# Optimization experiments

Hardware: AMD Instinct MI355X
Metric: run time of the kernel (lower is better)

The kernel has to match this reference:

```python
import jax, jax.numpy as jnp
import numpy as np

N = 50000      # nodes
E = 800000     # edges (avg degree 16)
LM = 768       # lm_input_dim
H = 192        # hidden_dim = 32*6
B6 = 32        # per-branch dim = hidden_dim/6
SLOPE = 0.01   # nn.LeakyReLU default negative slope


def setup_inputs() -> dict:
    key = jax.random.key(0)
    ks = jax.random.split(key, 32)
    f = lambda i, shape, s=0.05: (jax.random.normal(ks[i], shape, jnp.float32) * s)
    inp = {
        "pre_x": f(0, (N, LM)),
        "x": f(1, (N, LM)),
        "edge_index": jax.random.randint(ks[2], (2, E), 0, N),
        "edge_type": jax.random.randint(ks[3], (E,), 0, 3),
        "num_prop": f(4, (N, 5)),
        "num_category": f(5, (N, 1)),
        "des_tensor": f(6, (N, LM)),
        "tweet_tensor": f(7, (N, LM)),
        # parameters (torch nn.Linear convention: W is [out, in], y = x @ W.T + b)
        "W_des": f(8, (B6, LM)), "b_des": f(9, (B6,)),
        "W_tweet": f(10, (B6, LM)), "b_tweet": f(11, (B6,)),
        "W_tweet_tr": f(12, (B6, LM)), "b_tweet_tr": f(13, (B6,)),
        "W_prop": f(14, (B6, 5)), "b_prop": f(15, (B6,)),
        "W_cat": f(16, (B6, 1)), "b_cat": f(17, (B6,)),
        "W_text": f(18, (B6, LM)), "b_text": f(19, (B6,)),
        "W_in": f(20, (H, H)), "b_in": f(21, (H,)),
        "W_c1": f(22, (H, H)), "b_c1": f(23, (H,)),
        "W_c2": f(24, (H, H)), "b_c2": f(25, (H,)),
        "W_o1": f(26, (96, H)), "b_o1": f(27, (96,)),
        "W_o2": f(28, (2, 96)), "b_o2": f(29, (2,)),
    }
    return inp


def _gcn_conv(h, W, b, src, dst):
    """PyG GCNConv: symmetric-normalized aggregation with added self-loops.
    out[v] = sum_{u->v} (d_u d_v)^{-1/2} (h_u W^T) + (1/d_v) (h_v W^T) + b
    where d includes the self-loop (+1)."""
    n = h.shape[0]
    hW = h @ W.T                                                  # [N, H]
    deg = jax.ops.segment_sum(jnp.ones(src.shape[0], h.dtype), dst,
                              num_segments=n) + 1.0               # [N]
    dinv = jax.lax.rsqrt(deg)
    norm = dinv[src] * dinv[dst]                                  # [E]
    agg = jax.ops.segment_sum(hW[src] * norm[:, None], dst,
                              num_segments=n)                     # [N, H]
    return agg + hW * (1.0 / deg)[:, None] + b


def reference(pre_x, x, edge_index, edge_type, num_prop, num_category,
              des_tensor, tweet_tensor,
              W_des, b_des, W_tweet, b_tweet, W_tweet_tr, b_tweet_tr,
              W_prop, b_prop, W_cat, b_cat, W_text, b_text,
              W_in, b_in, W_c1, b_c1, W_c2, b_c2,
              W_o1, b_o1, W_o2, b_o2):
    lrelu = lambda v: jax.nn.leaky_relu(v, SLOPE)
    branch = lambda t, W, b: lrelu(t @ W.T + b)   # dropout is identity in eval

    d = branch(des_tensor, W_des, b_des)
    pre_t = branch(pre_x, W_tweet, b_tweet)
    t = branch(x, W_tweet_tr, b_tweet_tr)
    n = branch(num_prop, W_prop, b_prop)
    c = branch(num_category, W_cat, b_cat)
    tw = branch(tweet_tensor, W_text, b_text)

    h = jnp.concatenate((n, c, d, tw, pre_t, t), axis=1)          # [N, 192]
    h = lrelu(h @ W_in.T + b_in)

    src, dst = edge_index[0], edge_index[1]
    h = _gcn_conv(h, W_c1, b_c1, src, dst)
    h = _gcn_conv(h, W_c2, b_c2, src, dst)

    em = lrelu(h @ W_o1.T + b_o1)                                 # [N, 96]
    out = em @ W_o2.T + b_o2                                      # [N, 2]
    return (out, em)
```

## Files before the change

kernel.cpp:

```cpp
#include <hip/hip_runtime.h>

#define NN 50000
#define EE 800000
#define LMD 768
#define HD 192
#define SLOPE 0.01f

typedef short bf16x8 __attribute__((ext_vector_type(8)));
typedef float f32x4 __attribute__((ext_vector_type(4)));
typedef unsigned short u16;

__device__ __forceinline__ float lrelu(float v){ return v > 0.f ? v : SLOPE * v; }

__device__ __forceinline__ u16 f2bf(float f){
    unsigned u = __float_as_uint(f);
    u += 0x7FFF + ((u >> 16) & 1u);
    return (u16)(u >> 16);
}
__device__ __forceinline__ float bf2f(u16 v){
    return __uint_as_float(((unsigned)v) << 16);
}
__device__ __forceinline__ bf16x8 as_bf8(float4 v){
    union { float4 f; bf16x8 b; } u; u.f = v; return u.b;
}

__global__ __launch_bounds__(256) void k_prep(
    const float* __restrict__ W0, const float* __restrict__ W1,
    const float* __restrict__ W2, const float* __restrict__ W3,
    const float* __restrict__ Win, const float* __restrict__ Wc1,
    const float* __restrict__ Wc2, const float* __restrict__ Wo1,
    u16* __restrict__ out)
{
    int m = blockIdx.y;
    int idx = blockIdx.x * 256 + threadIdx.x;
    const float* src; int nelem; int K;
    switch (m) {
      case 0: src = W0;  nelem = 32*768;  K = 768; break;
      case 1: src = W1;  nelem = 32*768;  K = 768; break;
      case 2: src = W2;  nelem = 32*768;  K = 768; break;
      case 3: src = W3;  nelem = 32*768;  K = 768; break;
      case 4: src = Win; nelem = 192*192; K = 192; break;
      case 5: src = Wc1; nelem = 192*192; K = 192; break;
      case 6: src = Wc2; nelem = 192*192; K = 192; break;
      default: src = Wo1; nelem = 96*192; K = 192; break;
    }
    if (idx >= nelem) return;
    u16 v = f2bf(src[idx]);
    int c = idx / K, k = idx - c * K;
    int cb = c >> 4, lr = c & 15;
    int sg = k >> 5, kk = k & 31, hi = kk >> 3, j = kk & 7;
    int lane = hi * 16 + lr;
    size_t dst;
    if (m < 4)      dst = (size_t)m * 24576 + (sg * 2 + cb) * 512 + lane * 8 + j;
    else if (m < 7) dst = 98304 + (size_t)(m - 4) * 36864 + (sg * 12 + cb) * 512 + lane * 8 + j;
    else            dst = 208896 + (size_t)(sg * 6 + cb) * 512 + lane * 8 + j;
    out[dst] = v;
}

__global__ __launch_bounds__(256, 3) void k_branch(
    const float* __restrict__ des, const float* __restrict__ twt,
    const float* __restrict__ prex, const float* __restrict__ xx,
    const u16* __restrict__ Wf,
    const float* __restrict__ bd, const float* __restrict__ btx,
    const float* __restrict__ btw, const float* __restrict__ btr,
    u16* __restrict__ h)
{
    __shared__ u16 Abuf[16][776];
    __shared__ float scr[4][16][32];

    const int br = blockIdx.y;
    const float* A; const float* bias; int colBase;
    switch (br) {
      case 0:  A = des;  bias = bd;  colBase = 64;  break;
      case 1:  A = twt;  bias = btx; colBase = 96;  break;
      case 2:  A = prex; bias = btw; colBase = 128; break;
      default: A = xx;   bias = btr; colBase = 160; break;
    }

    const int t0 = threadIdx.x, w = t0 >> 6, l = t0 & 63;
    const int hi = l >> 4, lr = l & 15;

    bf16x8 Bfr[12];
    {
        const u16* wp = Wf + br * 24576;
        #pragma unroll
        for (int cc = 0; cc < 6; ++cc)
            #pragma unroll
            for (int cb = 0; cb < 2; ++cb)
                Bfr[cc * 2 + cb] = *(const bf16x8*)(wp + ((w * 6 + cc) * 2 + cb) * 512 + l * 8);
    }

    const int rrow = t0 >> 4;
    const int col0 = (t0 & 15) * 2;
    const float bias0 = bias[col0], bias1 = bias[col0 + 1];

    float4 f4[12];
    int tile = blockIdx.x;
    {
        const float* ab = A + (size_t)tile * 12288 + w * 3072 + l * 4;
        #pragma unroll
        for (int i = 0; i < 12; ++i) f4[i] = *(const float4*)(ab + i * 256);
    }

    for (; tile < 3125; tile += 192) {
        asm volatile("s_waitcnt vmcnt(0)" ::: "memory");
        #pragma unroll
        for (int i = 0; i < 12; ++i) {
            const int rr = i / 3, third = i % 3;
            unsigned plo = (unsigned)f2bf(f4[i].x) | ((unsigned)f2bf(f4[i].y) << 16);
            unsigned phi = (unsigned)f2bf(f4[i].z) | ((unsigned)f2bf(f4[i].w) << 16);
            uint2 pk; pk.x = plo; pk.y = phi;
            *(uint2*)&Abuf[w * 4 + rr][third * 256 + l * 4] = pk;
        }
        const int tnext = tile + 192;
        if (tnext < 3125) {
            const float* ab = A + (size_t)tnext * 12288 + w * 3072 + l * 4;
            #pragma unroll
            for (int i = 0; i < 12; ++i) f4[i] = *(const float4*)(ab + i * 256);
        }
        __syncthreads();

        f32x4 acc[2] = {};
        #pragma unroll
        for (int cc = 0; cc < 6; ++cc) {
            const int cg = w * 6 + cc;
            bf16x8 af = *(const bf16x8*)&Abuf[lr][cg * 32 + hi * 8];
            acc[0] = __builtin_amdgcn_mfma_f32_16x16x32_bf16(af, Bfr[cc * 2 + 0], acc[0], 0, 0, 0);
            acc[1] = __builtin_amdgcn_mfma_f32_16x16x32_bf16(af, Bfr[cc * 2 + 1], acc[1], 0, 0, 0);
        }
        #pragma unroll
        for (int cb = 0; cb < 2; ++cb)
            #pragma unroll
            for (int rg = 0; rg < 4; ++rg)
                scr[w][hi * 4 + rg][cb * 16 + lr] = acc[cb][rg];
        __syncthreads();

        float2 s; s.x = 0.f; s.y = 0.f;
        #pragma unroll
        for (int ww = 0; ww < 4; ++ww) {
            float2 p = *(const float2*)&scr[ww][rrow][col0];
            s.x += p.x; s.y += p.y;
        }
        float v0 = lrelu(s.x + bias0);
        float v1 = lrelu(s.y + bias1);
        unsigned pk = (unsigned)f2bf(v0) | ((unsigned)f2bf(v1) << 16);
        *(unsigned*)&h[((size_t)tile * 16 + rrow) * HD + colBase + col0] = pk;
    }
}

template<bool BIAS, bool LRELU>
__global__ __launch_bounds__(512) void k_hgemm(
    const u16* __restrict__ A, const u16* __restrict__ Wf,
    const float* __restrict__ bias, u16* __restrict__ out)
{
    __shared__ u16 Bs[36864];
    const int t = threadIdx.x, w = t >> 6, l = t & 63;
    const int hi = l >> 4, lr = l & 15;
    const int rowBase = blockIdx.x * 128;
    {
        const uint4* s_ = (const uint4*)Wf; uint4* d_ = (uint4*)Bs;
        #pragma unroll
        for (int i = 0; i < 9; ++i) d_[i * 512 + t] = s_[i * 512 + t];
    }
    int r0 = rowBase + w * 16 + lr;
    int rowc = r0 < NN ? r0 : NN - 1;
    const u16* ap = A + (size_t)rowc * HD;
    float4 araw[6];
    #pragma unroll
    for (int sg = 0; sg < 6; ++sg) {
        araw[sg] = *(const float4*)(ap + sg * 32 + hi * 8);
        asm volatile("" :: "v"(araw[sg].x), "v"(araw[sg].y), "v"(araw[sg].z), "v"(araw[sg].w));
    }
    __syncthreads();

    f32x4 acc[12] = {};
    #pragma unroll
    for (int sg = 0; sg < 6; ++sg) {
        bf16x8 af = as_bf8(araw[sg]);
        #pragma unroll
        for (int cb = 0; cb < 12; ++cb) {
            bf16x8 bf = *(const bf16x8*)(Bs + (sg * 12 + cb) * 512 + l * 8);
            acc[cb] = __builtin_amdgcn_mfma_f32_16x16x32_bf16(af, bf, acc[cb], 0, 0, 0);
        }
    }

    #pragma unroll
    for (int cb = 0; cb < 12; ++cb) {
        int cl = cb * 16 + lr;
        float bv = BIAS ? bias[cl] : 0.f;
        #pragma unroll
        for (int rg = 0; rg < 4; ++rg) {
            int r = rowBase + w * 16 + hi * 4 + rg;
            if (r < NN) {
                float v = acc[cb][rg] + bv;
                if (LRELU) v = lrelu(v);
                out[(size_t)r * HD + cl] = f2bf(v);
            }
        }
    }
}

__global__ __launch_bounds__(512) void k_final(
    const u16* __restrict__ A, const u16* __restrict__ Wf,
    const float* __restrict__ b1, const float* __restrict__ W2,
    const float* __restrict__ b2, float* __restrict__ em, float* __restrict__ out)
{
    __shared__ u16 Bs[18432];
    const int t = threadIdx.x, w = t >> 6, l = t & 63;
    const int hi = l >> 4, lr = l & 15;
    const int rowBase = blockIdx.x * 128;
    {
        const uint4* s_ = (const uint4*)Wf; uint4* d_ = (uint4*)Bs;
        #pragma unroll
        for (int i = 0; i < 5; ++i) { int idx = i * 512 + t; if (idx < 2304) d_[idx] = s_[idx]; }
    }
    int r0 = rowBase + w * 16 + lr;
    int rowc = r0 < NN ? r0 : NN - 1;
    const u16* ap = A + (size_t)rowc * HD;
    float4 araw[6];
    #pragma unroll
    for (int sg = 0; sg < 6; ++sg) {
        araw[sg] = *(const float4*)(ap + sg * 32 + hi * 8);
        asm volatile("" :: "v"(araw[sg].x), "v"(araw[sg].y), "v"(araw[sg].z), "v"(araw[sg].w));
    }
    __syncthreads();

    f32x4 acc[6] = {};
    #pragma unroll
    for (int sg = 0; sg < 6; ++sg) {
        bf16x8 af = as_bf8(araw[sg]);
        #pragma unroll
        for (int cb = 0; cb < 6; ++cb) {
            bf16x8 bf = *(const bf16x8*)(Bs + (sg * 6 + cb) * 512 + l * 8);
            acc[cb] = __builtin_amdgcn_mfma_f32_16x16x32_bf16(af, bf, acc[cb], 0, 0, 0);
        }
    }

    float w2v[2][6], bv[6];
    #pragma unroll
    for (int cb = 0; cb < 6; ++cb) {
        bv[cb] = b1[cb * 16 + lr];
        w2v[0][cb] = W2[cb * 16 + lr];
        w2v[1][cb] = W2[96 + cb * 16 + lr];
    }

    #pragma unroll
    for (int rg = 0; rg < 4; ++rg) {
        int r = rowBase + w * 16 + hi * 4 + rg;
        float o0 = 0.f, o1 = 0.f;
        #pragma unroll
        for (int cb = 0; cb < 6; ++cb) {
            float v = lrelu(acc[cb][rg] + bv[cb]);
            if (r < NN) em[(size_t)r * 96 + cb * 16 + lr] = v;
            o0 += v * w2v[0][cb];
            o1 += v * w2v[1][cb];
        }
        #pragma unroll
        for (int d = 1; d < 16; d <<= 1) {
            o0 += __shfl_xor(o0, d);
            o1 += __shfl_xor(o1, d);
        }
        if (lr == 0 && r < NN) {
            out[r * 2 + 0] = o0 + b2[0];
            out[r * 2 + 1] = o1 + b2[1];
        }
    }
}

__global__ __launch_bounds__(256) void k_small_branch(
    const float* __restrict__ nprop, const float* __restrict__ ncat,
    const float* __restrict__ Wp, const float* __restrict__ bp,
    const float* __restrict__ Wc, const float* __restrict__ bc,
    u16* __restrict__ h)
{
    int idx = blockIdx.x * 256 + threadIdx.x;
    if (idx >= NN * 64) return;
    int row = idx >> 6, c = idx & 63;
    float acc;
    if (c < 32) {
        acc = bp[c];
        #pragma unroll
        for (int k = 0; k < 5; ++k) acc += nprop[row * 5 + k] * Wp[c * 5 + k];
    } else {
        int cc = c - 32;
        acc = bc[cc] + ncat[row] * Wc[cc];
    }
    h[(size_t)row * HD + c] = f2bf(lrelu(acc));
}

__global__ void k_count(const int* __restrict__ ei, int* __restrict__ deg)
{
    int e = blockIdx.x * 256 + threadIdx.x;
    if (e < EE) atomicAdd(&deg[ei[EE + e]], 1);
}

__global__ void k_deginv(const int* __restrict__ deg, float* __restrict__ dinv, float* __restrict__ invdeg)
{
    int v = blockIdx.x * 256 + threadIdx.x;
    if (v < NN) {
        float d = (float)(deg[v] + 1);
        dinv[v] = rsqrtf(d);
        invdeg[v] = 1.0f / d;
    }
}

__global__ __launch_bounds__(1024) void k_scan1(const int* __restrict__ deg, int* __restrict__ rp, int* __restrict__ part)
{
    __shared__ int sh[1024];
    int tid = threadIdx.x, i = blockIdx.x * 1024 + tid;
    int x = (i < NN) ? deg[i] : 0;
    sh[tid] = x;
    __syncthreads();
    for (int off = 1; off < 1024; off <<= 1) {
        int y = (tid >= off) ? sh[tid - off] : 0;
        __syncthreads();
        sh[tid] += y;
        __syncthreads();
    }
    if (i < NN) rp[i] = sh[tid] - x;
    if (tid == 1023) part[blockIdx.x] = sh[tid];
}

__global__ void k_scan2(int* part, int nb, int* rp)
{
    if (threadIdx.x == 0 && blockIdx.x == 0) {
        int run = 0;
        for (int b = 0; b < nb; ++b) { int t = part[b]; part[b] = run; run += t; }
        rp[NN] = run;
    }
}

__global__ void k_scan3(int* rp, const int* __restrict__ part)
{
    int i = blockIdx.x * 256 + threadIdx.x;
    if (i < NN) rp[i] += part[i >> 10];
}

__global__ void k_fill(const int* __restrict__ ei, const float* __restrict__ dinv,
                       int* __restrict__ cursor, int* __restrict__ cs, float* __restrict__ nrm)
{
    int e = blockIdx.x * 256 + threadIdx.x;
    if (e >= EE) return;
    int s = ei[e], d = ei[EE + e];
    int pos = atomicAdd(&cursor[d], 1);
    cs[pos] = s;
    nrm[pos] = dinv[s] * dinv[d];
}

__global__ __launch_bounds__(240) void k_agg(const u16* __restrict__ hW,
    const int* __restrict__ rp, const int* __restrict__ cs, const float* __restrict__ nrm,
    const float* __restrict__ invdeg, const float* __restrict__ bias, u16* __restrict__ out)
{
    int v = blockIdx.x * 5 + threadIdx.y;
    int f0 = threadIdx.x * 4;
    int s0 = rp[v], s1 = rp[v + 1];
    float4 bv = *reinterpret_cast<const float4*>(bias + f0);
    ushort4 hv = *reinterpret_cast<const ushort4*>(hW + (size_t)v * HD + f0);
    float idg = invdeg[v];
    float a0 = bf2f(hv.x) * idg + bv.x;
    float a1 = bf2f(hv.y) * idg + bv.y;
    float a2 = bf2f(hv.z) * idg + bv.z;
    float a3 = bf2f(hv.w) * idg + bv.w;
    int i = s0;
    for (; i + 4 <= s1; i += 4) {
        int c0 = cs[i], c1 = cs[i+1], c2 = cs[i+2], c3 = cs[i+3];
        float n0 = nrm[i], n1 = nrm[i+1], n2 = nrm[i+2], n3 = nrm[i+3];
        ushort4 g0 = *reinterpret_cast<const ushort4*>(hW + (size_t)c0 * HD + f0);
        ushort4 g1 = *reinterpret_cast<const ushort4*>(hW + (size_t)c1 * HD + f0);
        ushort4 g2 = *reinterpret_cast<const ushort4*>(hW + (size_t)c2 * HD + f0);
        ushort4 g3 = *reinterpret_cast<const ushort4*>(hW + (size_t)c3 * HD + f0);
        a0 += bf2f(g0.x) * n0; a1 += bf2f(g0.y) * n0; a2 += bf2f(g0.z) * n0; a3 += bf2f(g0.w) * n0;
        a0 += bf2f(g1.x) * n1; a1 += bf2f(g1.y) * n1; a2 += bf2f(g1.z) * n1; a3 += bf2f(g1.w) * n1;
        a0 += bf2f(g2.x) * n2; a1 += bf2f(g2.y) * n2; a2 += bf2f(g2.z) * n2; a3 += bf2f(g2.w) * n2;
        a0 += bf2f(g3.x) * n3; a1 += bf2f(g3.y) * n3; a2 += bf2f(g3.z) * n3; a3 += bf2f(g3.w) * n3;
    }
    for (; i < s1; ++i) {
        int c = cs[i]; float n = nrm[i];
        ushort4 g = *reinterpret_cast<const ushort4*>(hW + (size_t)c * HD + f0);
        a0 += bf2f(g.x) * n; a1 += bf2f(g.y) * n; a2 += bf2f(g.z) * n; a3 += bf2f(g.w) * n;
    }
    ushort4 o;
    o.x = f2bf(a0); o.y = f2bf(a1); o.z = f2bf(a2); o.w = f2bf(a3);
    *reinterpret_cast<ushort4*>(out + (size_t)v * HD + f0) = o;
}

extern "C" void kernel_launch(void* const* d_in, const int* in_sizes, int n_in,
                              void* d_out, int out_size, void* d_ws, size_t ws_size,
                              hipStream_t stream)
{
    const float* pre_x = (const float*)d_in[0];
    const float* x     = (const float*)d_in[1];
    const int*   ei    = (const int*)d_in[2];
    const float* nprop = (const float*)d_in[4];
    const float* ncat  = (const float*)d_in[5];
    const float* des   = (const float*)d_in[6];
    const float* twt   = (const float*)d_in[7];
    const float* W_des  = (const float*)d_in[8],  *b_des  = (const float*)d_in[9];
    const float* W_tw   = (const float*)d_in[10], *b_tw   = (const float*)d_in[11];
    const float* W_tr   = (const float*)d_in[12], *b_tr   = (const float*)d_in[13];
    const float* W_prop = (const float*)d_in[14], *b_prop = (const float*)d_in[15];
    const float* W_cat  = (const float*)d_in[16], *b_cat  = (const float*)d_in[17];
    const float* W_text = (const float*)d_in[18], *b_text = (const float*)d_in[19];
    const float* W_in   = (const float*)d_in[20], *b_in   = (const float*)d_in[21];
    const float* W_c1   = (const float*)d_in[22], *b_c1   = (const float*)d_in[23];
    const float* W_c2   = (const float*)d_in[24], *b_c2   = (const float*)d_in[25];
    const float* W_o1   = (const float*)d_in[26], *b_o1   = (const float*)d_in[27];
    const float* W_o2   = (const float*)d_in[28], *b_o2   = (const float*)d_in[29];

    char* base = (char*)d_ws;
    size_t off = 0;
    auto alloc = [&](size_t bytes) -> char* {
        char* p = base + off;
        off = (off + bytes + 255) & ~(size_t)255;
        return p;
    };
    u16*   hA     = (u16*)alloc((size_t)NN * HD * 2);
    u16*   hB     = (u16*)alloc((size_t)NN * HD * 2);
    u16*   hC     = (u16*)alloc((size_t)NN * HD * 2);
    u16*   Wprep  = (u16*)alloc((size_t)227328 * 2);
    float* dinv   = (float*)alloc((size_t)NN * 4);
    float* invdeg = (float*)alloc((size_t)NN * 4);
    int*   deg    = (int*)alloc((size_t)NN * 4);
    int*   rp     = (int*)alloc((size_t)(NN + 1) * 4);
    int*   cursor = (int*)alloc((size_t)NN * 4);
    int*   part   = (int*)alloc(64 * 4);
    int*   cs     = (int*)alloc((size_t)EE * 4);
    float* nrm    = (float*)alloc((size_t)EE * 4);
    (void)ws_size; (void)in_sizes; (void)n_in; (void)out_size;

    float* outp = (float*)d_out;
    float* em   = outp + (size_t)NN * 2;

    const int rb     = (NN + 255) / 256;
    const int rb128  = (NN + 127) / 128;
    const int eb     = (EE + 255) / 256;
    const int nb1024 = (NN + 1023) / 1024;

    hipMemsetAsync(deg, 0, (size_t)NN * 4, stream);
    hipLaunchKernelGGL(k_prep, dim3(144, 8), dim3(256), 0, stream,
        W_des, W_text, W_tw, W_tr, W_in, W_c1, W_c2, W_o1, Wprep);
    hipLaunchKernelGGL(k_count,  dim3(eb), dim3(256), 0, stream, ei, deg);
    hipLaunchKernelGGL(k_deginv, dim3(rb), dim3(256), 0, stream, deg, dinv, invdeg);
    hipLaunchKernelGGL(k_scan1,  dim3(nb1024), dim3(1024), 0, stream, deg, rp, part);
    hipLaunchKernelGGL(k_scan2,  dim3(1), dim3(1), 0, stream, part, nb1024, rp);
    hipLaunchKernelGGL(k_scan3,  dim3(rb), dim3(256), 0, stream, rp, part);
    hipMemcpyAsync(cursor, rp, (size_t)NN * 4, hipMemcpyDeviceToDevice, stream);
    hipLaunchKernelGGL(k_fill,   dim3(eb), dim3(256), 0, stream, ei, dinv, cursor, cs, nrm);

    hipLaunchKernelGGL(k_branch, dim3(192, 4), dim3(256), 0, stream,
        des, twt, pre_x, x, Wprep, b_des, b_text, b_tw, b_tr, hA);
    hipLaunchKernelGGL(k_small_branch, dim3((NN * 64 + 255) / 256), dim3(256), 0, stream,
        nprop, ncat, W_prop, b_prop, W_cat, b_cat, hA);

    hipLaunchKernelGGL((k_hgemm<true, true>),   dim3(rb128), dim3(512), 0, stream,
        hA, Wprep + 98304, b_in, hB);
    hipLaunchKernelGGL((k_hgemm<false, false>), dim3(rb128), dim3(512), 0, stream,
        hB, Wprep + 98304 + 36864, nullptr, hC);
    hipLaunchKernelGGL(k_agg, dim3(NN / 5), dim3(48, 5), 0, stream, hC, rp, cs, nrm, invdeg, b_c1, hA);
    hipLaunchKernelGGL((k_hgemm<false, false>), dim3(rb128), dim3(512), 0, stream,
        hA, Wprep + 98304 + 2 * 36864, nullptr, hB);
    hipLaunchKernelGGL(k_agg, dim3(NN / 5), dim3(48, 5), 0, stream, hB, rp, cs, nrm, invdeg, b_c2, hC);

    hipLaunchKernelGGL(k_final, dim3(rb128), dim3(512), 0, stream,
        hC, Wprep + 208896, b_o1, W_o2, b_o2, em, outp);
}
```

Before: 399.1 us.

## Fuse small branches, degree-inverse, cursor copy, and back-to-back hidden GEMMs

Folds the numeric/category branch into the main branch kernel, computes dinv/invdeg inside the first scan pass, and writes the cursor copy directly from scan3 instead of a separate memcpy. Input projection and first conv GEMM are fused into one kernel that keeps the intermediate in swizzled LDS and reads weights straight from global. The branch grid grows from 192 to 256 blocks per branch with a higher occupancy bound. This removes several launches and one full intermediate round trip through memory. The fused GEMM reads weights from global/L2 rather than LDS and uses more registers.

```diff
diff --git a/kernel.cpp b/kernel.cpp
--- a/kernel.cpp
+++ b/kernel.cpp
@@ -57,12 +57,15 @@
     out[dst] = v;
 }
 
-__global__ __launch_bounds__(256, 3) void k_branch(
+__global__ __launch_bounds__(256, 4) void k_branch(
     const float* __restrict__ des, const float* __restrict__ twt,
     const float* __restrict__ prex, const float* __restrict__ xx,
     const u16* __restrict__ Wf,
     const float* __restrict__ bd, const float* __restrict__ btx,
     const float* __restrict__ btw, const float* __restrict__ btr,
+    const float* __restrict__ nprop, const float* __restrict__ ncat,
+    const float* __restrict__ Wp, const float* __restrict__ bp,
+    const float* __restrict__ Wc, const float* __restrict__ bc,
     u16* __restrict__ h)
 {
     __shared__ u16 Abuf[16][776];
@@ -102,17 +105,17 @@
         for (int i = 0; i < 12; ++i) f4[i] = *(const float4*)(ab + i * 256);
     }
 
-    for (; tile < 3125; tile += 192) {
+    for (; tile < 3125; tile += 256) {
         asm volatile("s_waitcnt vmcnt(0)" ::: "memory");
         #pragma unroll
         for (int i = 0; i < 12; ++i) {
             const int rr = i / 3, third = i % 3;
-            unsigned plo = (unsigned)f2bf(f4[i].x) | ((unsigned)f2bf(f4[i].y) << 16);
-            unsigned phi = (unsigned)f2bf(f4[i].z) | ((unsigned)f2bf(f4[i].w) << 16);
-            uint2 pk; pk.x = plo; pk.y = phi;
+            uint2 pk;
+            pk.x = (unsigned)f2bf(f4[i].x) | ((unsigned)f2bf(f4[i].y) << 16);
+            pk.y = (unsigned)f2bf(f4[i].z) | ((unsigned)f2bf(f4[i].w) << 16);
             *(uint2*)&Abuf[w * 4 + rr][third * 256 + l * 4] = pk;
         }
-        const int tnext = tile + 192;
+        const int tnext = tile + 256;
         if (tnext < 3125) {
             const float* ab = A + (size_t)tnext * 12288 + w * 3072 + l * 4;
             #pragma unroll
@@ -141,10 +144,98 @@
             float2 p = *(const float2*)&scr[ww][rrow][col0];
             s.x += p.x; s.y += p.y;
         }
-        float v0 = lrelu(s.x + bias0);
-        float v1 = lrelu(s.y + bias1);
-        unsigned pk = (unsigned)f2bf(v0) | ((unsigned)f2bf(v1) << 16);
+        unsigned pk = (unsigned)f2bf(lrelu(s.x + bias0)) | ((unsigned)f2bf(lrelu(s.y + bias1)) << 16);
         *(unsigned*)&h[((size_t)tile * 16 + rrow) * HD + colBase + col0] = pk;
+
+        if (br == 0) {
+            const int c0 = (t0 & 15) * 4;
+            const size_t row = (size_t)tile * 16 + rrow;
+            float o[4];
+            #pragma unroll
+            for (int j = 0; j < 4; ++j) {
+                int c = c0 + j;
+                float accv;
+                if (c < 32) {
+                    accv = bp[c];
+                    #pragma unroll
+                    for (int k = 0; k < 5; ++k) accv += nprop[row * 5 + k] * Wp[c * 5 + k];
+                } else {
+                    accv = bc[c - 32] + ncat[row] * Wc[c - 32];
+                }
+                o[j] = lrelu(accv);
+            }
+            uint2 pk2;
+            pk2.x = (unsigned)f2bf(o[0]) | ((unsigned)f2bf(o[1]) << 16);
+            pk2.y = (unsigned)f2bf(o[2]) | ((unsigned)f2bf(o[3]) << 16);
+            *(uint2*)&h[row * HD + c0] = pk2;
+        }
+    }
+}
+
+__global__ __launch_bounds__(512) void k_hgemm2(
+    const u16* __restrict__ A, const u16* __restrict__ Wf1, const u16* __restrict__ Wf2,
+    const float* __restrict__ b1, u16* __restrict__ out)
+{
+    __shared__ u16 h1s[128 * 192];
+    const int t = threadIdx.x, w = t >> 6, l = t & 63;
+    const int hi = l >> 4, lr = l & 15;
+    const int rowBase = blockIdx.x * 128;
+    int r0 = rowBase + w * 16 + lr;
+    int rowc = r0 < NN ? r0 : NN - 1;
+    const u16* ap = A + (size_t)rowc * HD;
+
+    bf16x8 afr[6];
+    #pragma unroll
+    for (int sg = 0; sg < 6; ++sg)
+        afr[sg] = *(const bf16x8*)(ap + sg * 32 + hi * 8);
+
+    f32x4 acc[12] = {};
+    #pragma unroll
+    for (int sg = 0; sg < 6; ++sg)
+        #pragma unroll
+        for (int cb = 0; cb < 12; ++cb) {
+            bf16x8 bf = *(const bf16x8*)(Wf1 + (sg * 12 + cb) * 512 + l * 8);
+            acc[cb] = __builtin_amdgcn_mfma_f32_16x16x32_bf16(afr[sg], bf, acc[cb], 0, 0, 0);
+        }
+
+    #pragma unroll
+    for (int cb = 0; cb < 12; ++cb) {
+        int cl = cb * 16 + lr;
+        float bv = b1[cl];
+        #pragma unroll
+        for (int rg = 0; rg < 4; ++rg) {
+            int rr = w * 16 + hi * 4 + rg;
+            int colp = (((cl >> 3) ^ (rr & 7)) << 3) | (cl & 7);
+            h1s[rr * 192 + colp] = f2bf(lrelu(acc[cb][rg] + bv));
+        }
+    }
+    __syncthreads();
+
+    int rr2 = w * 16 + lr;
+    bf16x8 af2[6];
+    #pragma unroll
+    for (int sg = 0; sg < 6; ++sg) {
+        int chunk = (sg * 4 + hi) ^ (rr2 & 7);
+        af2[sg] = *(const bf16x8*)&h1s[rr2 * 192 + chunk * 8];
+    }
+
+    f32x4 acc2[12] = {};
+    #pragma unroll
+    for (int sg = 0; sg < 6; ++sg)
+        #pragma unroll
+        for (int cb = 0; cb < 12; ++cb) {
+            bf16x8 bf = *(const bf16x8*)(Wf2 + (sg * 12 + cb) * 512 + l * 8);
+            acc2[cb] = __builtin_amdgcn_mfma_f32_16x16x32_bf16(af2[sg], bf, acc2[cb], 0, 0, 0);
+        }
+
+    #pragma unroll
+    for (int cb = 0; cb < 12; ++cb) {
+        int cl = cb * 16 + lr;
+        #pragma unroll
+        for (int rg = 0; rg < 4; ++rg) {
+            int r = rowBase + w * 16 + hi * 4 + rg;
+            if (r < NN) out[(size_t)r * HD + cl] = f2bf(acc2[cb][rg]);
+        }
     }
 }
 
@@ -267,48 +358,24 @@
     }
 }
 
-__global__ __launch_bounds__(256) void k_small_branch(
-    const float* __restrict__ nprop, const float* __restrict__ ncat,
-    const float* __restrict__ Wp, const float* __restrict__ bp,
-    const float* __restrict__ Wc, const float* __restrict__ bc,
-    u16* __restrict__ h)
-{
-    int idx = blockIdx.x * 256 + threadIdx.x;
-    if (idx >= NN * 64) return;
-    int row = idx >> 6, c = idx & 63;
-    float acc;
-    if (c < 32) {
-        acc = bp[c];
-        #pragma unroll
-        for (int k = 0; k < 5; ++k) acc += nprop[row * 5 + k] * Wp[c * 5 + k];
-    } else {
-        int cc = c - 32;
-        acc = bc[cc] + ncat[row] * Wc[cc];
-    }
-    h[(size_t)row * HD + c] = f2bf(lrelu(acc));
-}
-
 __global__ void k_count(const int* __restrict__ ei, int* __restrict__ deg)
 {
     int e = blockIdx.x * 256 + threadIdx.x;
     if (e < EE) atomicAdd(&deg[ei[EE + e]], 1);
 }
 
-__global__ void k_deginv(const int* __restrict__ deg, float* __restrict__ dinv, float* __restrict__ invdeg)
-{
-    int v = blockIdx.x * 256 + threadIdx.x;
-    if (v < NN) {
-        float d = (float)(deg[v] + 1);
-        dinv[v] = rsqrtf(d);
-        invdeg[v] = 1.0f / d;
-    }
-}
-
-__global__ __launch_bounds__(1024) void k_scan1(const int* __restrict__ deg, int* __restrict__ rp, int* __restrict__ part)
+__global__ __launch_bounds__(1024) void k_scan1(const int* __restrict__ deg, int* __restrict__ rp,
+                                                int* __restrict__ part,
+                                                float* __restrict__ dinv, float* __restrict__ invdeg)
 {
     __shared__ int sh[1024];
     int tid = threadIdx.x, i = blockIdx.x * 1024 + tid;
     int x = (i < NN) ? deg[i] : 0;
+    if (i < NN) {
+        float d = (float)(x + 1);
+        dinv[i] = rsqrtf(d);
+        invdeg[i] = 1.0f / d;
+    }
     sh[tid] = x;
     __syncthreads();
     for (int off = 1; off < 1024; off <<= 1) {
@@ -330,10 +397,14 @@
     }
 }
 
-__global__ void k_scan3(int* rp, const int* __restrict__ part)
+__global__ void k_scan3(int* rp, const int* __restrict__ part, int* __restrict__ cursor)
 {
     int i = blockIdx.x * 256 + threadIdx.x;
-    if (i < NN) rp[i] += part[i >> 10];
+    if (i < NN) {
+        int v = rp[i] + part[i >> 10];
+        rp[i] = v;
+        cursor[i] = v;
+    }
 }
 
 __global__ void k_fill(const int* __restrict__ ei, const float* __restrict__ dinv,
@@ -440,27 +511,22 @@
     hipLaunchKernelGGL(k_prep, dim3(144, 8), dim3(256), 0, stream,
         W_des, W_text, W_tw, W_tr, W_in, W_c1, W_c2, W_o1, Wprep);
     hipLaunchKernelGGL(k_count,  dim3(eb), dim3(256), 0, stream, ei, deg);
-    hipLaunchKernelGGL(k_deginv, dim3(rb), dim3(256), 0, stream, deg, dinv, invdeg);
-    hipLaunchKernelGGL(k_scan1,  dim3(nb1024), dim3(1024), 0, stream, deg, rp, part);
+    hipLaunchKernelGGL(k_scan1,  dim3(nb1024), dim3(1024), 0, stream, deg, rp, part, dinv, invdeg);
     hipLaunchKernelGGL(k_scan2,  dim3(1), dim3(1), 0, stream, part, nb1024, rp);
-    hipLaunchKernelGGL(k_scan3,  dim3(rb), dim3(256), 0, stream, rp, part);
-    hipMemcpyAsync(cursor, rp, (size_t)NN * 4, hipMemcpyDeviceToDevice, stream);
+    hipLaunchKernelGGL(k_scan3,  dim3(rb), dim3(256), 0, stream, rp, part, cursor);
     hipLaunchKernelGGL(k_fill,   dim3(eb), dim3(256), 0, stream, ei, dinv, cursor, cs, nrm);
 
-    hipLaunchKernelGGL(k_branch, dim3(192, 4), dim3(256), 0, stream,
-        des, twt, pre_x, x, Wprep, b_des, b_text, b_tw, b_tr, hA);
-    hipLaunchKernelGGL(k_small_branch, dim3((NN * 64 + 255) / 256), dim3(256), 0, stream,
+    hipLaunchKernelGGL(k_branch, dim3(256, 4), dim3(256), 0, stream,
+        des, twt, pre_x, x, Wprep, b_des, b_text, b_tw, b_tr,
         nprop, ncat, W_prop, b_prop, W_cat, b_cat, hA);
 
-    hipLaunchKernelGGL((k_hgemm<true, true>),   dim3(rb128), dim3(512), 0, stream,
-        hA, Wprep + 98304, b_in, hB);
+    hipLaunchKernelGGL(k_hgemm2, dim3(rb128), dim3(512), 0, stream,
+        hA, Wprep + 98304, Wprep + 98304 + 36864, b_in, hB);
+    hipLaunchKernelGGL(k_agg, dim3(NN / 5), dim3(48, 5), 0, stream, hB, rp, cs, nrm, invdeg, b_c1, hC);
     hipLaunchKernelGGL((k_hgemm<false, false>), dim3(rb128), dim3(512), 0, stream,
-        hB, Wprep + 98304 + 36864, nullptr, hC);
-    hipLaunchKernelGGL(k_agg, dim3(NN / 5), dim3(48, 5), 0, stream, hC, rp, cs, nrm, invdeg, b_c1, hA);
-    hipLaunchKernelGGL((k_hgemm<false, false>), dim3(rb128), dim3(512), 0, stream,
-        hA, Wprep + 98304 + 2 * 36864, nullptr, hB);
-    hipLaunchKernelGGL(k_agg, dim3(NN / 5), dim3(48, 5), 0, stream, hB, rp, cs, nrm, invdeg, b_c2, hC);
+        hC, Wprep + 98304 + 2 * 36864, nullptr, hA);
+    hipLaunchKernelGGL(k_agg, dim3(NN / 5), dim3(48, 5), 0, stream, hA, rp, cs, nrm, invdeg, b_c2, hB);
 
     hipLaunchKernelGGL(k_final, dim3(rb128), dim3(512), 0, stream,
-        hC, Wprep + 208896, b_o1, W_o2, b_o2, em, outp);
-}
+        hB, Wprep + 208896, b_o1, W_o2, b_o2, em, outp);
+}
```

After: 460.3 us. 1.15x slower.
